# Optimization experiments

Hardware: AMD Instinct MI355X
Metric: run time of the kernel (lower is better)

The kernel has to match this reference:

```python
import jax, jax.numpy as jnp
import numpy as np
from jax import lax

DN = ('NCHW', 'OIHW', 'NCHW')

def _hard_sigmoid(x):
    return jnp.clip(0.2 * x + 0.5, 0.0, 1.0)

def _conv(x, k, pad):
    return lax.conv_general_dilated(x, k, (1, 1), pad, dimension_numbers=DN)

def setup_inputs() -> dict:
    key = jax.random.key(0)
    k1, k2, k3 = jax.random.split(key, 3)
    B, T, C, H, W = 8, 16, 8, 128, 128
    F = 32
    x = jax.random.normal(k1, (B, T, C, H, W), dtype=jnp.float32)
    Wk = jax.random.normal(k2, (4 * F, C, 3, 3), dtype=jnp.float32) * 0.05
    Uk = jax.random.normal(k3, (4 * F, F, 3, 3), dtype=jnp.float32) * 0.05
    b = jnp.zeros((4 * F,), dtype=jnp.float32)
    return {"x": x, "Wk": Wk, "Uk": Uk, "b": b}

def reference(x, Wk, Uk, b):
    # ConvLSTM2D, channels_first, valid padding on input conv, same on recurrent conv,
    # gate order i,f,c,o; activation=tanh, recurrent_activation=hard_sigmoid.
    B, T, C, H, W = x.shape
    F = Uk.shape[1]
    kh, kw = Wk.shape[2], Wk.shape[3]
    Ho, Wo = H - kh + 1, W - kw + 1  # valid padding output spatial size
    bias = b[None, :, None, None]

    def step(carry, xt):
        h, c = carry
        z = _conv(xt, Wk, 'VALID') + _conv(h, Uk, 'SAME') + bias  # [B,4F,Ho,Wo]
        i, f, g, o = jnp.split(z, 4, axis=1)
        i = _hard_sigmoid(i)
        f = _hard_sigmoid(f)
        o = _hard_sigmoid(o)
        c_new = f * c + i * jnp.tanh(g)
        h_new = o * jnp.tanh(c_new)
        return (h_new, c_new), None

    h0 = jnp.zeros((B, F, Ho, Wo), dtype=x.dtype)
    c0 = jnp.zeros((B, F, Ho, Wo), dtype=x.dtype)
    xs = jnp.transpose(x, (1, 0, 2, 3, 4))  # [T,B,C,H,W]
    (hT, cT), _ = lax.scan(step, (h0, c0), xs)
    return hT  # return_sequences=False -> final hidden state [B,F,Ho,Wo]
```

## Files before the change

kernel.cpp:

```cpp
#include <hip/hip_runtime.h>
#include <hip/hip_bf16.h>

typedef __bf16 bf16_t;
typedef __attribute__((ext_vector_type(8))) __bf16 bf16x8;
typedef __attribute__((ext_vector_type(4))) __bf16 bf16x4;
typedef __attribute__((ext_vector_type(16))) float f32x16;
typedef unsigned int u32;

#define B_ 8
#define T_ 16
#define C_ 8
#define F_ 32
#define H_ 128
#define W_ 128
#define HO 126
#define WO 126

#define XS_OFF 0
#define HS_OFF 2880
#define BB_OFF 14400
#define LDS_BYTES 22592
#define NKK 23

__global__ __launch_bounds__(256) void prep_B(const float* __restrict__ Wk,
                                              const float* __restrict__ Uk,
                                              bf16_t* __restrict__ Bp) {
    int e = blockIdx.x * 256 + threadIdx.x;
    int j = e & 7, lane = (e >> 3) & 63, nt = (e >> 9) & 3, kk = e >> 11;
    int n = nt * 32 + (lane & 31), half = lane >> 5;
    float v = 0.f;
    if (kk < 5) {
        int p = 2 * kk + half, c = j;
        if (p <= 8) v = Wk[((n * C_ + c) * 3 + p / 3) * 3 + (p % 3)];
    } else {
        int kk2 = kk - 5, q = kk2 >> 1;
        int f = ((kk2 & 1) << 4) + (half << 3) + j;
        v = Uk[((n * F_ + f) * 3 + q / 3) * 3 + (q % 3)];
    }
    Bp[e] = (bf16_t)v;
}

__global__ __launch_bounds__(256, 3) void lstm_step(
    const float* __restrict__ x, int t,
    const bf16_t* __restrict__ Bp,
    const float* __restrict__ bias,
    const float* __restrict__ h_in,
    float* __restrict__ c_st,
    float* __restrict__ h_out)
{
    __shared__ __align__(16) unsigned char smem[LDS_BYTES];
    const int tid = threadIdx.x;
    const int w = tid >> 6, l = tid & 63;
    const int bx = blockIdx.x, by = blockIdx.y, bb = blockIdx.z;
    const int r0 = by * 8, c0 = bx * 16;

    const float* xb = x + (size_t)(bb * T_ + t) * (C_ * H_ * W_);
    for (int i = tid; i < 1440; i += 256) {
        int c = i / 180, rem = i % 180;
        int row = rem / 18, col = rem % 18;
        int gy = r0 + row, gx = c0 + col;
        float v = 0.f;
        if (gy < H_ && gx < W_) v = xb[(c * H_ + gy) * W_ + gx];
        *(bf16_t*)(smem + XS_OFF + row * 288 + col * 16 + c * 2) = (bf16_t)v;
    }
    const float* hb = h_in + (size_t)bb * (HO * WO * F_);
    for (int i = tid; i < 1440; i += 256) {
        int pix = i >> 3, fq = i & 7;
        int row = pix / 18, col = pix % 18;
        int gy = r0 - 1 + row, gx = c0 - 1 + col;
        float4 v = make_float4(0.f, 0.f, 0.f, 0.f);
        if (gy >= 0 && gy < HO && gx >= 0 && gx < WO)
            v = *(const float4*)(hb + (size_t)(gy * WO + gx) * F_ + fq * 4);
        bf16x4 pv = {(bf16_t)v.x, (bf16_t)v.y, (bf16_t)v.z, (bf16_t)v.w};
        *(bf16x4*)(smem + HS_OFF + (fq >> 1) * 2880 + row * 288 + col * 16 + (fq & 1) * 8) = pv;
    }

    const int fch = l & 31, half = l >> 5;
    const int rtA = (l >> 4) & 1, colA = l & 15;
    const int rt_full = 2 * w + rtA;
    const int baseX = rt_full * 288 + colA * 16;
    const int baseH = HS_OFF + half * 2880 + baseX;
    const int baseB = BB_OFF + l * 16;

    f32x16 acc[4];
    #pragma unroll
    for (int nt = 0; nt < 4; ++nt) {
        float bv = bias[nt * 32 + fch];
        #pragma unroll
        for (int j = 0; j < 16; ++j) acc[nt][j] = bv;
    }

    {
        const unsigned char* src = (const unsigned char*)Bp + (w << 10) + l * 16;
        __builtin_amdgcn_global_load_lds((const __attribute__((address_space(1))) u32*)src,
            (__attribute__((address_space(3))) u32*)(smem + BB_OFF + (w << 10)), 16, 0, 0);
    }
    __syncthreads();

    constexpr int OFFP[10] = {0, 16, 32, 288, 304, 320, 576, 592, 608, 864};

    #pragma unroll
    for (int kk = 0; kk < NKK; ++kk) {
        if (kk + 1 < NKK) {
            const unsigned char* src =
                (const unsigned char*)Bp + (((kk + 1) * 4 + w) << 10) + l * 16;
            __builtin_amdgcn_global_load_lds((const __attribute__((address_space(1))) u32*)src,
                (__attribute__((address_space(3))) u32*)(smem + BB_OFF + (((kk + 1) & 1) << 12) + (w << 10)),
                16, 0, 0);
        }
        int aoff;
        if (kk < 5) {
            aoff = baseX + (half ? OFFP[2 * kk + 1] : OFFP[2 * kk]);
        } else {
            const int kk2 = kk - 5, q = kk2 >> 1;
            aoff = baseH + (kk2 & 1) * 5760 + (q / 3) * 288 + (q % 3) * 16;
        }
        bf16x8 av = *(const bf16x8*)(smem + aoff);
        const int bbs = baseB + ((kk & 1) << 12);
        bf16x8 b0 = *(const bf16x8*)(smem + bbs);
        bf16x8 b1 = *(const bf16x8*)(smem + bbs + 1024);
        bf16x8 b2 = *(const bf16x8*)(smem + bbs + 2048);
        bf16x8 b3 = *(const bf16x8*)(smem + bbs + 3072);
        acc[0] = __builtin_amdgcn_mfma_f32_32x32x16_bf16(av, b0, acc[0], 0, 0, 0);
        acc[1] = __builtin_amdgcn_mfma_f32_32x32x16_bf16(av, b1, acc[1], 0, 0, 0);
        acc[2] = __builtin_amdgcn_mfma_f32_32x32x16_bf16(av, b2, acc[2], 0, 0, 0);
        acc[3] = __builtin_amdgcn_mfma_f32_32x32x16_bf16(av, b3, acc[3], 0, 0, 0);
        __syncthreads();
    }

    float* cb = c_st + (size_t)bb * (HO * WO * F_);
    float* ho = h_out + (size_t)bb * (HO * WO * F_);
    #pragma unroll
    for (int r = 0; r < 16; ++r) {
        const int m = (r & 3) + ((r >> 2) << 3) + (half << 2);
        const int gy = r0 + 2 * w + (m >> 4), gx = c0 + (m & 15);
        if (gy < HO && gx < WO) {
            const int pidx = (gy * WO + gx) * F_ + fch;
            float zi = acc[0][r], zf = acc[1][r], zg = acc[2][r], zo = acc[3][r];
            float ig = fminf(fmaxf(0.2f * zi + 0.5f, 0.f), 1.f);
            float fg = fminf(fmaxf(0.2f * zf + 0.5f, 0.f), 1.f);
            float og = fminf(fmaxf(0.2f * zo + 0.5f, 0.f), 1.f);
            float eg = __expf(2.f * zg);
            float tg = 1.f - 2.f / (eg + 1.f);
            float cn = fg * cb[pidx] + ig * tg;
            cb[pidx] = cn;
            float ec = __expf(2.f * cn);
            ho[pidx] = og * (1.f - 2.f / (ec + 1.f));
        }
    }
}

__global__ __launch_bounds__(256) void out_transpose(const float* __restrict__ h,
                                                     float* __restrict__ out) {
    __shared__ float tile[WO * 33];
    const int gy = blockIdx.x, bb = blockIdx.y;
    const float* hp = h + ((size_t)bb * HO + gy) * (WO * F_);
    for (int i = threadIdx.x; i < WO * F_; i += 256) {
        int gx = i >> 5, f = i & 31;
        tile[gx * 33 + f] = hp[i];
    }
    __syncthreads();
    float* op = out + (size_t)bb * (F_ * HO * WO) + (size_t)gy * WO;
    for (int i = threadIdx.x; i < WO * F_; i += 256) {
        int f = i / WO, gx = i % WO;
        op[(size_t)f * (HO * WO) + gx] = tile[gx * 33 + f];
    }
}

extern "C" void kernel_launch(void* const* d_in, const int* in_sizes, int n_in,
                              void* d_out, int out_size, void* d_ws, size_t ws_size,
                              hipStream_t stream) {
    const float* x    = (const float*)d_in[0];
    const float* Wk   = (const float*)d_in[1];
    const float* Uk   = (const float*)d_in[2];
    const float* bias = (const float*)d_in[3];
    float* out = (float*)d_out;

    const size_t N = (size_t)B_ * HO * WO * F_;
    float* h0 = (float*)d_ws;
    float* h1 = h0 + N;
    float* c  = h1 + N;
    bf16_t* Bp = (bf16_t*)(c + N);

    hipMemsetAsync(h0, 0, N * sizeof(float), stream);
    hipMemsetAsync(c, 0, N * sizeof(float), stream);
    prep_B<<<184, 256, 0, stream>>>(Wk, Uk, Bp);

    dim3 grid(8, 16, B_);
    for (int t = 0; t < T_; ++t) {
        const float* hin = (t & 1) ? h1 : h0;
        float* hout = (t & 1) ? h0 : h1;
        lstm_step<<<grid, 256, 0, stream>>>(x, t, Bp, bias, hin, c, hout);
    }
    out_transpose<<<dim3(HO, B_), 256, 0, stream>>>(h0, out);
}
```

Baseline: 537.5 us.

## Replace per-timestep launches with persistent cooperative kernel and bf16 state

Replaces the 16 per-timestep kernel launches with one persistent cooperative kernel of 256 blocks that loops over time and synchronises through an atomic grid barrier. The cell state stays in registers across steps, all weights stay resident in LDS, and each block computes a larger 32x16 tile with two A fragments per weight load. The input is pre-converted to a bf16 channels-last buffer and h is stored in bf16, which halves state traffic. The costs are spin-wait barrier overhead, a bounded spin that can time out and leave a race, extra precision loss from storing h in bf16, and lower occupancy from the large LDS footprint.

```diff
diff --git a/kernel.cpp b/kernel.cpp
--- a/kernel.cpp
+++ b/kernel.cpp
@@ -3,9 +3,7 @@
 
 typedef __bf16 bf16_t;
 typedef __attribute__((ext_vector_type(8))) __bf16 bf16x8;
-typedef __attribute__((ext_vector_type(4))) __bf16 bf16x4;
 typedef __attribute__((ext_vector_type(16))) float f32x16;
-typedef unsigned int u32;
 
 #define B_ 8
 #define T_ 16
@@ -15,12 +13,13 @@
 #define W_ 128
 #define HO 126
 #define WO 126
-
-#define XS_OFF 0
-#define HS_OFF 2880
-#define BB_OFF 14400
-#define LDS_BYTES 22592
 #define NKK 23
+#define NBLK 256
+
+#define BQ (NKK * 4096)
+#define XS_OFF BQ
+#define HS_OFF (BQ + 9792)
+#define LDS_BYTES (BQ + 9792 + 39168)
 
 __global__ __launch_bounds__(256) void prep_B(const float* __restrict__ Wk,
                                               const float* __restrict__ Uk,
@@ -40,124 +39,182 @@
     Bp[e] = (bf16_t)v;
 }
 
-__global__ __launch_bounds__(256, 3) void lstm_step(
-    const float* __restrict__ x, int t,
+__global__ __launch_bounds__(128) void conv_x(const float* __restrict__ x,
+                                              bf16_t* __restrict__ xb) {
+    const int tx = threadIdx.x;
+    const int y = blockIdx.x, tb = blockIdx.y, bb = blockIdx.z;
+    const float* xp = x + ((size_t)(bb * T_ + tb) * C_) * (H_ * W_) + y * W_ + tx;
+    bf16x8 v;
+    #pragma unroll
+    for (int c = 0; c < 8; ++c) v[c] = (bf16_t)xp[(size_t)c * (H_ * W_)];
+    *(bf16x8*)(xb + (((size_t)(bb * T_ + tb) * H_ + y) * W_ + tx) * 8) = v;
+}
+
+__global__ __launch_bounds__(512, 2) void lstm_persist(
+    const bf16_t* __restrict__ xb,
     const bf16_t* __restrict__ Bp,
     const float* __restrict__ bias,
-    const float* __restrict__ h_in,
-    float* __restrict__ c_st,
-    float* __restrict__ h_out)
+    bf16_t* __restrict__ h0,
+    bf16_t* __restrict__ h1,
+    float* __restrict__ cbuf,
+    int* __restrict__ bar,
+    int t0, int nsteps)
 {
     __shared__ __align__(16) unsigned char smem[LDS_BYTES];
     const int tid = threadIdx.x;
     const int w = tid >> 6, l = tid & 63;
-    const int bx = blockIdx.x, by = blockIdx.y, bb = blockIdx.z;
-    const int r0 = by * 8, c0 = bx * 16;
-
-    const float* xb = x + (size_t)(bb * T_ + t) * (C_ * H_ * W_);
-    for (int i = tid; i < 1440; i += 256) {
-        int c = i / 180, rem = i % 180;
-        int row = rem / 18, col = rem % 18;
-        int gy = r0 + row, gx = c0 + col;
-        float v = 0.f;
-        if (gy < H_ && gx < W_) v = xb[(c * H_ + gy) * W_ + gx];
-        *(bf16_t*)(smem + XS_OFF + row * 288 + col * 16 + c * 2) = (bf16_t)v;
-    }
-    const float* hb = h_in + (size_t)bb * (HO * WO * F_);
-    for (int i = tid; i < 1440; i += 256) {
-        int pix = i >> 3, fq = i & 7;
-        int row = pix / 18, col = pix % 18;
-        int gy = r0 - 1 + row, gx = c0 - 1 + col;
-        float4 v = make_float4(0.f, 0.f, 0.f, 0.f);
-        if (gy >= 0 && gy < HO && gx >= 0 && gx < WO)
-            v = *(const float4*)(hb + (size_t)(gy * WO + gx) * F_ + fq * 4);
-        bf16x4 pv = {(bf16_t)v.x, (bf16_t)v.y, (bf16_t)v.z, (bf16_t)v.w};
-        *(bf16x4*)(smem + HS_OFF + (fq >> 1) * 2880 + row * 288 + col * 16 + (fq & 1) * 8) = pv;
-    }
-
-    const int fch = l & 31, half = l >> 5;
-    const int rtA = (l >> 4) & 1, colA = l & 15;
-    const int rt_full = 2 * w + rtA;
-    const int baseX = rt_full * 288 + colA * 16;
-    const int baseH = HS_OFF + half * 2880 + baseX;
-    const int baseB = BB_OFF + l * 16;
-
-    f32x16 acc[4];
-    #pragma unroll
-    for (int nt = 0; nt < 4; ++nt) {
-        float bv = bias[nt * 32 + fch];
-        #pragma unroll
-        for (int j = 0; j < 16; ++j) acc[nt][j] = bv;
-    }
-
-    {
-        const unsigned char* src = (const unsigned char*)Bp + (w << 10) + l * 16;
-        __builtin_amdgcn_global_load_lds((const __attribute__((address_space(1))) u32*)src,
-            (__attribute__((address_space(3))) u32*)(smem + BB_OFF + (w << 10)), 16, 0, 0);
-    }
-    __syncthreads();
-
-    constexpr int OFFP[10] = {0, 16, 32, 288, 304, 320, 576, 592, 608, 864};
-
-    #pragma unroll
-    for (int kk = 0; kk < NKK; ++kk) {
-        if (kk + 1 < NKK) {
-            const unsigned char* src =
-                (const unsigned char*)Bp + (((kk + 1) * 4 + w) << 10) + l * 16;
-            __builtin_amdgcn_global_load_lds((const __attribute__((address_space(1))) u32*)src,
-                (__attribute__((address_space(3))) u32*)(smem + BB_OFF + (((kk + 1) & 1) << 12) + (w << 10)),
-                16, 0, 0);
-        }
-        int aoff;
-        if (kk < 5) {
-            aoff = baseX + (half ? OFFP[2 * kk + 1] : OFFP[2 * kk]);
-        } else {
-            const int kk2 = kk - 5, q = kk2 >> 1;
-            aoff = baseH + (kk2 & 1) * 5760 + (q / 3) * 288 + (q % 3) * 16;
-        }
-        bf16x8 av = *(const bf16x8*)(smem + aoff);
-        const int bbs = baseB + ((kk & 1) << 12);
-        bf16x8 b0 = *(const bf16x8*)(smem + bbs);
-        bf16x8 b1 = *(const bf16x8*)(smem + bbs + 1024);
-        bf16x8 b2 = *(const bf16x8*)(smem + bbs + 2048);
-        bf16x8 b3 = *(const bf16x8*)(smem + bbs + 3072);
-        acc[0] = __builtin_amdgcn_mfma_f32_32x32x16_bf16(av, b0, acc[0], 0, 0, 0);
-        acc[1] = __builtin_amdgcn_mfma_f32_32x32x16_bf16(av, b1, acc[1], 0, 0, 0);
-        acc[2] = __builtin_amdgcn_mfma_f32_32x32x16_bf16(av, b2, acc[2], 0, 0, 0);
-        acc[3] = __builtin_amdgcn_mfma_f32_32x32x16_bf16(av, b3, acc[3], 0, 0, 0);
+    const int half = l >> 5;
+    const int bid = blockIdx.x;
+    const int bx = bid & 7, by = (bid >> 3) & 3, bb = bid >> 5;
+    const int r0 = by * 32, c0 = bx * 16;
+
+    for (int i = tid; i < BQ / 16; i += 512)
+        *(bf16x8*)(smem + i * 16) = *(const bf16x8*)(Bp + i * 8);
+
+    const int fch = l & 31;
+    float bv[4];
+    #pragma unroll
+    for (int n = 0; n < 4; ++n) bv[n] = bias[n * 32 + fch];
+
+    const int trA = w * 4 + ((l & 31) >> 4);
+    const int tcA = l & 15;
+    const int baseX0 = XS_OFF + trA * 288 + tcA * 16;
+    const int baseH0 = HS_OFF + half * 9792 + trA * 288 + tcA * 16;
+
+    float* cbp = cbuf + (size_t)bb * (HO * WO * F_);
+    float cre[2][16];
+    #pragma unroll
+    for (int m = 0; m < 2; ++m)
+        #pragma unroll
+        for (int r = 0; r < 16; ++r) {
+            const int row = (r & 3) + ((r >> 2) << 3) + (half << 2);
+            const int px = w * 64 + m * 32 + row;
+            const int gy = r0 + (px >> 4), gx = c0 + (px & 15);
+            cre[m][r] = (gy < HO && gx < WO) ? cbp[((size_t)gy * WO + gx) * F_ + fch] : 0.f;
+        }
+
+    constexpr int OFFT[10] = {0, 16, 32, 288, 304, 320, 576, 592, 608, 864};
+
+    #pragma unroll 1
+    for (int ts = 0; ts < nsteps; ++ts) {
+        const int t = t0 + ts;
+        const bf16_t* hr = (t & 1) ? h1 : h0;
+        bf16_t* hw = (t & 1) ? h0 : h1;
+
+        const bf16_t* xt = xb + (size_t)(bb * T_ + t) * (H_ * W_ * 8);
+        for (int i = tid; i < 612; i += 512) {
+            int row = i / 18, col = i % 18;
+            int gy = r0 + row, gx = c0 + col;
+            bf16x8 v = {};
+            if (gy < H_ && gx < W_) v = *(const bf16x8*)(xt + ((size_t)gy * W_ + gx) * 8);
+            *(bf16x8*)(smem + XS_OFF + row * 288 + col * 16) = v;
+        }
+        const bf16_t* hbR = hr + (size_t)bb * (HO * WO * F_);
+        for (int i = tid; i < 2448; i += 512) {
+            int pix = i >> 2, fg = i & 3;
+            int row = pix / 18, col = pix % 18;
+            int gy = r0 - 1 + row, gx = c0 - 1 + col;
+            bf16x8 v = {};
+            if (gy >= 0 && gy < HO && gx >= 0 && gx < WO)
+                v = *(const bf16x8*)(hbR + ((size_t)gy * WO + gx) * F_ + fg * 8);
+            *(bf16x8*)(smem + HS_OFF + fg * 9792 + row * 288 + col * 16) = v;
+        }
         __syncthreads();
-    }
-
-    float* cb = c_st + (size_t)bb * (HO * WO * F_);
-    float* ho = h_out + (size_t)bb * (HO * WO * F_);
-    #pragma unroll
-    for (int r = 0; r < 16; ++r) {
-        const int m = (r & 3) + ((r >> 2) << 3) + (half << 2);
-        const int gy = r0 + 2 * w + (m >> 4), gx = c0 + (m & 15);
-        if (gy < HO && gx < WO) {
-            const int pidx = (gy * WO + gx) * F_ + fch;
-            float zi = acc[0][r], zf = acc[1][r], zg = acc[2][r], zo = acc[3][r];
-            float ig = fminf(fmaxf(0.2f * zi + 0.5f, 0.f), 1.f);
-            float fg = fminf(fmaxf(0.2f * zf + 0.5f, 0.f), 1.f);
-            float og = fminf(fmaxf(0.2f * zo + 0.5f, 0.f), 1.f);
-            float eg = __expf(2.f * zg);
-            float tg = 1.f - 2.f / (eg + 1.f);
-            float cn = fg * cb[pidx] + ig * tg;
-            cb[pidx] = cn;
-            float ec = __expf(2.f * cn);
-            ho[pidx] = og * (1.f - 2.f / (ec + 1.f));
-        }
-    }
-}
-
-__global__ __launch_bounds__(256) void out_transpose(const float* __restrict__ h,
+
+        f32x16 acc[2][4];
+        #pragma unroll
+        for (int m = 0; m < 2; ++m)
+            #pragma unroll
+            for (int n = 0; n < 4; ++n)
+                #pragma unroll
+                for (int j = 0; j < 16; ++j) acc[m][n][j] = bv[n];
+
+        #pragma unroll
+        for (int kk = 0; kk < NKK; ++kk) {
+            int base0;
+            if (kk < 5) {
+                base0 = baseX0 + (half ? OFFT[2 * kk + 1] : OFFT[2 * kk]);
+            } else {
+                const int kk2 = kk - 5, q = kk2 >> 1, fgrp = kk2 & 1;
+                base0 = baseH0 + fgrp * 19584 + (q / 3) * 288 + (q % 3) * 16;
+            }
+            bf16x8 a0 = *(const bf16x8*)(smem + base0);
+            bf16x8 a1 = *(const bf16x8*)(smem + base0 + 576);
+            const int bbo = kk * 4096 + l * 16;
+            bf16x8 b0 = *(const bf16x8*)(smem + bbo);
+            bf16x8 b1 = *(const bf16x8*)(smem + bbo + 1024);
+            bf16x8 b2 = *(const bf16x8*)(smem + bbo + 2048);
+            bf16x8 b3 = *(const bf16x8*)(smem + bbo + 3072);
+            acc[0][0] = __builtin_amdgcn_mfma_f32_32x32x16_bf16(a0, b0, acc[0][0], 0, 0, 0);
+            acc[0][1] = __builtin_amdgcn_mfma_f32_32x32x16_bf16(a0, b1, acc[0][1], 0, 0, 0);
+            acc[0][2] = __builtin_amdgcn_mfma_f32_32x32x16_bf16(a0, b2, acc[0][2], 0, 0, 0);
+            acc[0][3] = __builtin_amdgcn_mfma_f32_32x32x16_bf16(a0, b3, acc[0][3], 0, 0, 0);
+            acc[1][0] = __builtin_amdgcn_mfma_f32_32x32x16_bf16(a1, b0, acc[1][0], 0, 0, 0);
+            acc[1][1] = __builtin_amdgcn_mfma_f32_32x32x16_bf16(a1, b1, acc[1][1], 0, 0, 0);
+            acc[1][2] = __builtin_amdgcn_mfma_f32_32x32x16_bf16(a1, b2, acc[1][2], 0, 0, 0);
+            acc[1][3] = __builtin_amdgcn_mfma_f32_32x32x16_bf16(a1, b3, acc[1][3], 0, 0, 0);
+        }
+
+        bf16_t* hwb = hw + (size_t)bb * (HO * WO * F_);
+        #pragma unroll
+        for (int m = 0; m < 2; ++m)
+            #pragma unroll
+            for (int r = 0; r < 16; ++r) {
+                const int row = (r & 3) + ((r >> 2) << 3) + (half << 2);
+                const int px = w * 64 + m * 32 + row;
+                const int gy = r0 + (px >> 4), gx = c0 + (px & 15);
+                float zi = acc[m][0][r], zf = acc[m][1][r], zg = acc[m][2][r], zo = acc[m][3][r];
+                float ig = fminf(fmaxf(0.2f * zi + 0.5f, 0.f), 1.f);
+                float fg = fminf(fmaxf(0.2f * zf + 0.5f, 0.f), 1.f);
+                float og = fminf(fmaxf(0.2f * zo + 0.5f, 0.f), 1.f);
+                float eg = __expf(2.f * zg);
+                float tg = 1.f - 2.f / (eg + 1.f);
+                float cn = fg * cre[m][r] + ig * tg;
+                cre[m][r] = cn;
+                float ec = __expf(2.f * cn);
+                float hn = og * (1.f - 2.f / (ec + 1.f));
+                if (gy < HO && gx < WO)
+                    hwb[((size_t)gy * WO + gx) * F_ + fch] = (bf16_t)hn;
+            }
+
+        if (ts < nsteps - 1) {
+            __threadfence();
+            __syncthreads();
+            if (tid == 0) {
+                atomicAdd(&bar[t], 1);
+                int it = 0;
+                while (__hip_atomic_load(&bar[t], __ATOMIC_ACQUIRE,
+                                         __HIP_MEMORY_SCOPE_AGENT) < NBLK &&
+                       it < (1 << 13)) {
+                    __builtin_amdgcn_s_sleep(4);
+                    ++it;
+                }
+            }
+            __syncthreads();
+            __threadfence();
+        }
+    }
+
+    #pragma unroll
+    for (int m = 0; m < 2; ++m)
+        #pragma unroll
+        for (int r = 0; r < 16; ++r) {
+            const int row = (r & 3) + ((r >> 2) << 3) + (half << 2);
+            const int px = w * 64 + m * 32 + row;
+            const int gy = r0 + (px >> 4), gx = c0 + (px & 15);
+            if (gy < HO && gx < WO)
+                cbp[((size_t)gy * WO + gx) * F_ + fch] = cre[m][r];
+        }
+}
+
+__global__ __launch_bounds__(256) void out_transpose(const bf16_t* __restrict__ h,
                                                      float* __restrict__ out) {
     __shared__ float tile[WO * 33];
     const int gy = blockIdx.x, bb = blockIdx.y;
-    const float* hp = h + ((size_t)bb * HO + gy) * (WO * F_);
+    const bf16_t* hp = h + ((size_t)bb * HO + gy) * (WO * F_);
     for (int i = threadIdx.x; i < WO * F_; i += 256) {
         int gx = i >> 5, f = i & 31;
-        tile[gx * 33 + f] = hp[i];
+        tile[gx * 33 + f] = (float)hp[i];
     }
     __syncthreads();
     float* op = out + (size_t)bb * (F_ * HO * WO) + (size_t)gy * WO;
@@ -177,20 +234,31 @@
     float* out = (float*)d_out;
 
     const size_t N = (size_t)B_ * HO * WO * F_;
-    float* h0 = (float*)d_ws;
-    float* h1 = h0 + N;
-    float* c  = h1 + N;
-    bf16_t* Bp = (bf16_t*)(c + N);
-
-    hipMemsetAsync(h0, 0, N * sizeof(float), stream);
-    hipMemsetAsync(c, 0, N * sizeof(float), stream);
+    bf16_t* h0p  = (bf16_t*)d_ws;
+    bf16_t* h1p  = h0p + N;
+    bf16_t* Bp   = h1p + N;
+    bf16_t* xbuf = Bp + 47104;
+    float*  cbuf = (float*)(xbuf + (size_t)16777216);
+    int*    bar  = (int*)(cbuf + N);
+
+    conv_x<<<dim3(H_, T_, B_), 128, 0, stream>>>(x, xbuf);
     prep_B<<<184, 256, 0, stream>>>(Wk, Uk, Bp);
-
-    dim3 grid(8, 16, B_);
-    for (int t = 0; t < T_; ++t) {
-        const float* hin = (t & 1) ? h1 : h0;
-        float* hout = (t & 1) ? h0 : h1;
-        lstm_step<<<grid, 256, 0, stream>>>(x, t, Bp, bias, hin, c, hout);
-    }
-    out_transpose<<<dim3(HO, B_), 256, 0, stream>>>(h0, out);
-}
+    hipMemsetAsync(h0p, 0, N * sizeof(bf16_t), stream);
+    hipMemsetAsync(cbuf, 0, N * sizeof(float), stream);
+    hipMemsetAsync(bar, 0, 16 * sizeof(int), stream);
+
+    int t0 = 0, ns = T_;
+    const bf16_t* xbc = xbuf;
+    const bf16_t* Bpc = Bp;
+    void* args[] = {(void*)&xbc, (void*)&Bpc, (void*)&bias, (void*)&h0p,
+                    (void*)&h1p, (void*)&cbuf, (void*)&bar, (void*)&t0, (void*)&ns};
+    hipError_t ce = hipLaunchCooperativeKernel((const void*)lstm_persist,
+                                               dim3(NBLK), dim3(512), args, 0, stream);
+    if (ce != hipSuccess) {
+        for (int t = 0; t < T_; ++t)
+            lstm_persist<<<NBLK, 512, 0, stream>>>(xbuf, Bp, bias, h0p, h1p,
+                                                   cbuf, bar, t, 1);
+    }
+
+    out_transpose<<<dim3(HO, B_), 256, 0, stream>>>(h0p, out);
+}
```

After: 2.144 ms. 3.99x slower.
